# Kernel optimization log

Measured on AMD Instinct MI355X. Metric: run time of the kernel, lower is better.

## Reference

```python
import jax, jax.numpy as jnp
import numpy as np

E, B, S, D, F = 8, 2, 1024, 1024, 4096


def setup_inputs() -> dict:
    key = jax.random.key(0)
    ks = jax.random.split(key, 9)
    sc_d = 1.0 / np.sqrt(D)
    sc_f = 1.0 / np.sqrt(F)
    hidden_states = jax.random.normal(ks[0], (B, S, D), dtype=jnp.float32)
    # router outputs set externally on the parent model in the original code
    gating_probs = jax.nn.softmax(jax.random.normal(ks[1], (B, E), dtype=jnp.float32), axis=-1)
    shared_gate_prob = jax.nn.sigmoid(jax.random.normal(ks[2], (B, 1), dtype=jnp.float32))
    # stacked expert SwiGLU MLP weights (Llama-style gate/up/down)
    Wg = jax.random.normal(ks[3], (E, D, F), dtype=jnp.float32) * sc_d
    Wu = jax.random.normal(ks[4], (E, D, F), dtype=jnp.float32) * sc_d
    Wd = jax.random.normal(ks[5], (E, F, D), dtype=jnp.float32) * sc_f
    # shared expert MLP
    Sg = jax.random.normal(ks[6], (D, F), dtype=jnp.float32) * sc_d
    Su = jax.random.normal(ks[7], (D, F), dtype=jnp.float32) * sc_d
    Sd = jax.random.normal(ks[8], (F, D), dtype=jnp.float32) * sc_f
    return {
        "hidden_states": hidden_states,
        "gating_probs": gating_probs,
        "shared_gate_prob": shared_gate_prob,
        "Wg": Wg, "Wu": Wu, "Wd": Wd,
        "Sg": Sg, "Su": Su, "Sd": Sd,
    }


def reference(hidden_states, gating_probs, shared_gate_prob, Wg, Wu, Wd, Sg, Su, Sd):
    h = hidden_states  # [B,S,D]
    # every expert's MLP runs on all tokens (naive all-experts-dense, as in source)
    g = jnp.einsum("bsd,edf->ebsf", h, Wg)
    u = jnp.einsum("bsd,edf->ebsf", h, Wu)
    expert_outs = jnp.einsum("ebsf,efd->ebsd", jax.nn.silu(g) * u, Wd)  # [E,B,S,D]
    # weighted_sum routing with per-sequence gating probs [B,E]
    expert_output = jnp.einsum("be,ebsd->bsd", gating_probs, expert_outs)
    # shared expert MLP
    shared = jnp.einsum("bsf,fd->bsd", jax.nn.silu(h @ Sg) * (h @ Su), Sd)
    sg = shared_gate_prob[:, :, None]  # [B,1,1]
    return (1.0 - sg) * expert_output + sg * shared
```

## Files before the change

### kernel.cpp

```cpp
#include <hip/hip_runtime.h>
#include <cstdio>
#include <cstdint>

typedef _Float16 f16;
typedef _Float16 f16x4 __attribute__((ext_vector_type(4)));
typedef _Float16 f16x8 __attribute__((ext_vector_type(8)));
typedef float f32x4 __attribute__((ext_vector_type(4)));

#define GLL16(gp, lp)                                                          \
  __builtin_amdgcn_global_load_lds(                                            \
      (const __attribute__((address_space(1))) void*)(gp),                     \
      (__attribute__((address_space(3))) void*)(lp), 16, 0, 0)

#define BARX __builtin_amdgcn_s_barrier()
#define WAITV4 { asm volatile("s_waitcnt vmcnt(4)" ::: "memory"); __builtin_amdgcn_sched_barrier(0); }
#define WAITV0 { asm volatile("s_waitcnt vmcnt(0)" ::: "memory"); __builtin_amdgcn_sched_barrier(0); }
#define WAITL0 { asm volatile("s_waitcnt lgkmcnt(0)" ::: "memory"); __builtin_amdgcn_sched_barrier(0); }

__global__ void cvt_f32_f16_kernel(const float* __restrict__ in,
                                   f16* __restrict__ out, int n4) {
  int i = blockIdx.x * blockDim.x + threadIdx.x;
  if (i < n4) {
    f32x4 v = reinterpret_cast<const f32x4*>(in)[i];
    f16x4 o;
    o[0] = (f16)v[0]; o[1] = (f16)v[1]; o[2] = (f16)v[2]; o[3] = (f16)v[3];
    reinterpret_cast<f16x4*>(out)[i] = o;
  }
}

__global__ void tr_cvt2_kernel(const float* __restrict__ inA,
                               const float* __restrict__ inB,
                               f16* __restrict__ out, size_t slotOff,
                               int C, size_t OS, int nA) {
  int slot = blockIdx.z;
  const float* src = (slot < nA) ? inA + (size_t)slot * 64 * gridDim.y * C : inB;
  f16* dst = out + (size_t)slot * slotOff;
  __shared__ f16 tl[4096];
  int t = threadIdx.x;
  int r0 = blockIdx.y * 64, c0 = blockIdx.x * 64;
  int br = (t >> 4) * 4, bc = (t & 15) * 4;
  f32x4 v[4];
#pragma unroll
  for (int i = 0; i < 4; ++i)
    v[i] = *(const f32x4*)&src[(size_t)(r0 + br + i) * C + c0 + bc];
#pragma unroll
  for (int cc = 0; cc < 4; ++cc) {
    int c = bc + cc;
    f16x4 o;
    o[0] = (f16)v[0][cc]; o[1] = (f16)v[1][cc];
    o[2] = (f16)v[2][cc]; o[3] = (f16)v[3][cc];
    *(f16x4*)&tl[c * 64 + (br ^ ((c & 7) * 8))] = o;
  }
  __syncthreads();
  int rw = (t & 7) * 8, cw = t >> 3;
#pragma unroll
  for (int j = 0; j < 2; ++j) {
    int c = cw + j * 32;
    f16x8 o = *(const f16x8*)&tl[c * 64 + (rw ^ ((c & 7) * 8))];
    *(f16x8*)&dst[(size_t)(c0 + c) * OS + r0 + rw] = o;
  }
}

#define STAGE_A5(tile, hf)                                                     \
  do {                                                                         \
    const f16* g_ = Abase + (size_t)((hf) * 128) * 1024 + (tile) * 64 + aVoff; \
    f16* d_ = &lds[(2 * ((tile) & 1) + (hf)) * 8192 + w * 512];                \
    GLL16(g_, d_);                                                             \
    GLL16(g_ + (size_t)64 * 1024, d_ + 4096);                                  \
  } while (0)
#define STAGE_G5(tile)                                                         \
  do {                                                                         \
    const f16* g_ = Gbase + (tile) * 64 + aVoff;                               \
    f16* d_ = &lds[32768 + (2 * ((tile) & 1)) * 8192 + w * 512];               \
    GLL16(g_, d_);                                                             \
    GLL16(g_ + (size_t)64 * 1024, d_ + 4096);                                  \
  } while (0)
#define STAGE_U5(tile)                                                         \
  do {                                                                         \
    const f16* g_ = Ubase + (tile) * 64 + aVoff;                               \
    f16* d_ = &lds[32768 + (2 * ((tile) & 1) + 1) * 8192 + w * 512];           \
    GLL16(g_, d_);                                                             \
    GLL16(g_ + (size_t)64 * 1024, d_ + 4096);                                  \
  } while (0)

#define RD_A5(rh, buf)                                                         \
  do {                                                                         \
    const f16* p_ = &lds[(2 * (buf) + wr) * 8192 + (rh) * 4096];               \
    aFd[0][0] = *(const f16x8*)(p_ + 0 * 1024 + vR0);                          \
    aFd[0][1] = *(const f16x8*)(p_ + 0 * 1024 + vR1);                          \
    aFd[1][0] = *(const f16x8*)(p_ + 1 * 1024 + vR0);                          \
    aFd[1][1] = *(const f16x8*)(p_ + 1 * 1024 + vR1);                          \
    aFd[2][0] = *(const f16x8*)(p_ + 2 * 1024 + vR0);                          \
    aFd[2][1] = *(const f16x8*)(p_ + 2 * 1024 + vR1);                          \
    aFd[3][0] = *(const f16x8*)(p_ + 3 * 1024 + vR0);                          \
    aFd[3][1] = *(const f16x8*)(p_ + 3 * 1024 + vR1);                          \
  } while (0)
#define RD_B5(ch, buf)                                                         \
  do {                                                                         \
    const f16* p_ = &lds[32768 + (2 * (buf) + bh) * 8192 + bq * 4096 +         \
                         (ch) * 2 * 1024];                                     \
    bFd[(ch) * 2][0] = *(const f16x8*)(p_ + vR0);                              \
    bFd[(ch) * 2][1] = *(const f16x8*)(p_ + vR1);                              \
    bFd[(ch) * 2 + 1][0] = *(const f16x8*)(p_ + 1024 + vR0);                   \
    bFd[(ch) * 2 + 1][1] = *(const f16x8*)(p_ + 1024 + vR1);                   \
  } while (0)

#define MFMA165(rh, ch)                                                        \
  do {                                                                         \
    __builtin_amdgcn_s_setprio(1);                                             \
    _Pragma("unroll") for (int rt = 0; rt < 4; ++rt)                           \
        _Pragma("unroll") for (int ct = 0; ct < 2; ++ct)                       \
        _Pragma("unroll") for (int ks = 0; ks < 2; ++ks)                       \
            acc[(rh) * 4 + rt][(ch) * 2 + ct] =                                \
        __builtin_amdgcn_mfma_f32_16x16x32_f16(                                \
            aFd[rt][ks], bFd[(ch) * 2 + ct][ks],                               \
            acc[(rh) * 4 + rt][(ch) * 2 + ct], 0, 0, 0);                       \
    __builtin_amdgcn_s_setprio(0);                                             \
    __builtin_amdgcn_sched_barrier(0);                                         \
  } while (0)

__global__ __launch_bounds__(512, 2) void gemmUG5_kernel(
    const f16* __restrict__ A, const f16* __restrict__ Bg,
    const f16* __restrict__ Bu, f16* __restrict__ T,
    const float* __restrict__ gate, const float* __restrict__ sgp) {
  __shared__ __align__(16) f16 lds[65536];

  int lgl = (blockIdx.x & 7) * 288 + (blockIdx.x >> 3);
  int mt = lgl & 7;
  int ntg = lgl >> 3;
  int slot = ntg >> 5;
  int ntl = ntg & 31;

  int t = threadIdx.x, w = t >> 6, l = t & 63;
  int wr = w >> 2, wc = w & 3;
  int bh = wc >> 1, bq = wc & 1;

  int scol = (((l & 7) ^ ((l >> 3) & 7)) * 8);
  size_t aVoff = (size_t)(w * 8 + (l >> 3)) * 1024 + scol;
  const f16* Abase = A + (size_t)mt * 256 * 1024;
  const f16* Gbase = Bg + (size_t)slot * 4194304 + (size_t)ntl * 128 * 1024;
  const f16* Ubase = Bu + (size_t)slot * 4194304 + (size_t)ntl * 128 * 1024;

  int vR0 = (l & 15) * 64 + (((l >> 4) * 8) ^ ((l & 7) * 8));
  int vR1 = (l & 15) * 64 + ((32 + (l >> 4) * 8) ^ ((l & 7) * 8));

  f16x8 aFd[4][2], bFd[4][2];
  f32x4 acc[8][4] = {};

  STAGE_G5(0); STAGE_U5(0);
  STAGE_A5(0, 0); STAGE_A5(0, 1);
  STAGE_G5(1); STAGE_U5(1);
  WAITV4;
  BARX;

#pragma unroll 1
  for (int it = 0; it < 7; ++it) {
    int t1 = 2 * it + 1, t2 = 2 * it + 2, t3 = 2 * it + 3;
    RD_A5(0, 0); RD_B5(0, 0); STAGE_A5(t1, 0);
    BARX; WAITL0; MFMA165(0, 0); BARX;
    RD_B5(1, 0); STAGE_A5(t1, 1);
    BARX; WAITL0; MFMA165(0, 1); BARX;
    RD_A5(1, 0); STAGE_G5(t2);
    BARX; WAITL0; MFMA165(1, 0); BARX;
    STAGE_U5(t2);
    BARX; MFMA165(1, 1); WAITV4; BARX;
    RD_A5(0, 1); RD_B5(0, 1); STAGE_A5(t2, 0);
    BARX; WAITL0; MFMA165(0, 0); BARX;
    RD_B5(1, 1); STAGE_A5(t2, 1);
    BARX; WAITL0; MFMA165(0, 1); BARX;
    RD_A5(1, 1); STAGE_G5(t3);
    BARX; WAITL0; MFMA165(1, 0); BARX;
    STAGE_U5(t3);
    BARX; MFMA165(1, 1); WAITV4; BARX;
  }
  RD_A5(0, 0); RD_B5(0, 0); STAGE_A5(15, 0);
  BARX; WAITL0; MFMA165(0, 0); BARX;
  RD_B5(1, 0); STAGE_A5(15, 1);
  BARX; WAITL0; MFMA165(0, 1); BARX;
  RD_A5(1, 0);
  BARX; WAITL0; MFMA165(1, 0); BARX;
  BARX; MFMA165(1, 1); WAITV0; BARX;
  RD_A5(0, 1); RD_B5(0, 1);
  BARX; WAITL0; MFMA165(0, 0); BARX;
  RD_B5(1, 1);
  BARX; WAITL0; MFMA165(0, 1); BARX;
  RD_A5(1, 1);
  BARX; WAITL0; MFMA165(1, 0); BARX;
  MFMA165(1, 1);

  int r0 = (l >> 4) * 4, c0 = l & 15;
  float* xf = (float*)lds;
  if (wc >= 2) {
    float* wb = xf + (wr * 2 + (wc - 2)) * 8192 + l * 128;
#pragma unroll
    for (int rt = 0; rt < 8; ++rt)
#pragma unroll
      for (int ct = 0; ct < 4; ++ct)
        *(f32x4*)(wb + ((rt ^ (l & 7)) * 16 + ct * 4)) = acc[rt][ct];
  }
  WAITL0;
  BARX;
  if (wc < 2) {
    const float* rb = xf + (wr * 2 + wc) * 8192 + l * 128;
    int rowb = mt * 256 + wr * 128;
    size_t colb = (size_t)ntg * 128 + wc * 64;
    int b = mt >> 2;
    float s = sgp[b];
    float coef = (slot < 8) ? (1.f - s) * gate[b * 8 + slot] : s;
#pragma unroll
    for (int rt = 0; rt < 8; ++rt) {
#pragma unroll
      for (int ct = 0; ct < 4; ++ct) {
        f32x4 uv = *(const f32x4*)(rb + ((rt ^ (l & 7)) * 16 + ct * 4));
#pragma unroll
        for (int j = 0; j < 4; ++j) {
          float g = acc[rt][ct][j];
          float u = uv[j];
          T[(size_t)(rowb + rt * 16 + r0 + j) * 36864 + colb + ct * 16 + c0] =
              (f16)(g / (1.f + __expf(-g)) * u * coef);
        }
      }
    }
  }
}

#define STAGE_A(tile, hf)                                                      \
  do {                                                                         \
    const f16* g_ = Abase + (size_t)((hf) * 128) * LD + (tile) * 64 + aVoff;   \
    f16* d_ = &lds[(2 * ((tile) & 1) + (hf)) * 8192 + w * 512];                \
    GLL16(g_, d_);                                                             \
    GLL16(g_ + (size_t)64 * LD, d_ + 4096);                                    \
  } while (0)
#define STAGE_B(tile, hf)                                                      \
  do {                                                                         \
    const f16* g_ = Bbase + (size_t)((hf) * 128) * LD + (tile) * 64 + aVoff;   \
    f16* d_ = &lds[32768 + (2 * ((tile) & 1) + (hf)) * 8192 + w * 512];        \
    GLL16(g_, d_);                                                             \
    GLL16(g_ + (size_t)64 * LD, d_ + 4096);                                    \
  } while (0)

#define RD_A(rh, buf)                                                          \
  do {                                                                         \
    const f16* p_ = &lds[(2 * (buf) + wr) * 8192 + (rh) * 4096];               \
    aFd[0][0] = *(const f16x8*)(p_ + 0 * 1024 + vR0);                          \
    aFd[0][1] = *(const f16x8*)(p_ + 0 * 1024 + vR1);                          \
    aFd[1][0] = *(const f16x8*)(p_ + 1 * 1024 + vR0);                          \
    aFd[1][1] = *(const f16x8*)(p_ + 1 * 1024 + vR1);                          \
    aFd[2][0] = *(const f16x8*)(p_ + 2 * 1024 + vR0);                          \
    aFd[2][1] = *(const f16x8*)(p_ + 2 * 1024 + vR1);                          \
    aFd[3][0] = *(const f16x8*)(p_ + 3 * 1024 + vR0);                          \
    aFd[3][1] = *(const f16x8*)(p_ + 3 * 1024 + vR1);                          \
  } while (0)
#define RD_B(ch, buf)                                                          \
  do {                                                                         \
    const f16* p_ = &lds[32768 + (2 * (buf) + bh) * 8192 + bq * 4096 +         \
                         (ch) * 2 * 1024];                                     \
    bFd[(ch) * 2][0] = *(const f16x8*)(p_ + vR0);                              \
    bFd[(ch) * 2][1] = *(const f16x8*)(p_ + vR1);                              \
    bFd[(ch) * 2 + 1][0] = *(const f16x8*)(p_ + 1024 + vR0);                   \
    bFd[(ch) * 2 + 1][1] = *(const f16x8*)(p_ + 1024 + vR1);                   \
  } while (0)

#define MFMA16(rh, ch)                                                         \
  do {                                                                         \
    __builtin_amdgcn_s_setprio(1);                                             \
    _Pragma("unroll") for (int rt = 0; rt < 4; ++rt)                           \
        _Pragma("unroll") for (int ct = 0; ct < 2; ++ct)                       \
        _Pragma("unroll") for (int ks = 0; ks < 2; ++ks)                       \
            acc[(rh) * 4 + rt][(ch) * 2 + ct] =                                \
        __builtin_amdgcn_mfma_f32_16x16x32_f16(                                \
            aFd[rt][ks], bFd[(ch) * 2 + ct][ks],                               \
            acc[(rh) * 4 + rt][(ch) * 2 + ct], 0, 0, 0);                       \
    __builtin_amdgcn_s_setprio(0);                                             \
    __builtin_amdgcn_sched_barrier(0);                                         \
  } while (0)

__global__ __launch_bounds__(512, 2) void gemmD_kernel(
    const f16* __restrict__ A, const f16* __restrict__ B,
    float* __restrict__ P) {
  constexpr size_t LD = 36864;
  constexpr int NTILES = 72;
  __shared__ __align__(16) f16 lds[65536];

  int wg = (blockIdx.x & 7) * 32 + (blockIdx.x >> 3);
  int kpart = wg >> 5, mt = (wg >> 2) & 7, nt = wg & 3;

  int t = threadIdx.x, w = t >> 6, l = t & 63;
  int wr = w >> 2, wc = w & 3;
  int bh = wc >> 1, bq = wc & 1;

  int scol = (((l & 7) ^ ((l >> 3) & 7)) * 8);
  size_t stRow = (size_t)(w * 8 + (l >> 3)) * LD;
  size_t aVoff = stRow + scol;
  const f16* Abase = A + (size_t)mt * 256 * LD + (size_t)kpart * 4608;
  const f16* Bbase = B + (size_t)nt * 256 * LD + (size_t)kpart * 4608;

  int vR0 = (l & 15) * 64 + (((l >> 4) * 8) ^ ((l & 7) * 8));
  int vR1 = (l & 15) * 64 + ((32 + (l >> 4) * 8) ^ ((l & 7) * 8));

  f16x8 aFd[4][2], bFd[4][2];
  f32x4 acc[8][4] = {};

  STAGE_B(0, 0); STAGE_B(0, 1);
  STAGE_A(0, 0); STAGE_A(0, 1);
  STAGE_B(1, 0); STAGE_B(1, 1);
  WAITV4;
  BARX;

#pragma unroll 1
  for (int it = 0; it < NTILES / 2 - 1; ++it) {
    int t1 = 2 * it + 1, t2 = 2 * it + 2, t3 = 2 * it + 3;
    RD_A(0, 0); RD_B(0, 0); STAGE_A(t1, 0);
    BARX; WAITL0; MFMA16(0, 0); BARX;
    RD_B(1, 0); STAGE_A(t1, 1);
    BARX; WAITL0; MFMA16(0, 1); BARX;
    RD_A(1, 0); STAGE_B(t2, 0);
    BARX; WAITL0; MFMA16(1, 0); BARX;
    STAGE_B(t2, 1);
    BARX; MFMA16(1, 1); WAITV4; BARX;
    RD_A(0, 1); RD_B(0, 1); STAGE_A(t2, 0);
    BARX; WAITL0; MFMA16(0, 0); BARX;
    RD_B(1, 1); STAGE_A(t2, 1);
    BARX; WAITL0; MFMA16(0, 1); BARX;
    RD_A(1, 1); STAGE_B(t3, 0);
    BARX; WAITL0; MFMA16(1, 0); BARX;
    STAGE_B(t3, 1);
    BARX; MFMA16(1, 1); WAITV4; BARX;
  }
  RD_A(0, 0); RD_B(0, 0); STAGE_A(NTILES - 1, 0);
  BARX; WAITL0; MFMA16(0, 0); BARX;
  RD_B(1, 0); STAGE_A(NTILES - 1, 1);
  BARX; WAITL0; MFMA16(0, 1); BARX;
  RD_A(1, 0);
  BARX; WAITL0; MFMA16(1, 0); BARX;
  BARX; MFMA16(1, 1); WAITV0; BARX;
  RD_A(0, 1); RD_B(0, 1);
  BARX; WAITL0; MFMA16(0, 0); BARX;
  RD_B(1, 1);
  BARX; WAITL0; MFMA16(0, 1); BARX;
  RD_A(1, 1);
  BARX; WAITL0; MFMA16(1, 0); BARX;
  MFMA16(1, 1);

  int r0 = (l >> 4) * 4, c0 = l & 15;
  size_t base = ((size_t)kpart << 21);
  int rowbase = mt * 256 + wr * 128;
  int colbase = nt * 256 + wc * 64;
#pragma unroll
  for (int rt = 0; rt < 8; ++rt)
#pragma unroll
    for (int ct = 0; ct < 4; ++ct)
#pragma unroll
      for (int j = 0; j < 4; ++j)
        P[base + (size_t)(rowbase + rt * 16 + r0 + j) * 1024 + colbase +
          ct * 16 + c0] = acc[rt][ct][j];
}

__global__ void reduce8_kernel(const float* __restrict__ P,
                               float* __restrict__ out, int n4) {
  int i = blockIdx.x * blockDim.x + threadIdx.x;
  if (i < n4) {
    f32x4 s = {0.f, 0.f, 0.f, 0.f};
#pragma unroll
    for (int e = 0; e < 8; ++e) {
      f32x4 v = reinterpret_cast<const f32x4*>(P + ((size_t)e << 21))[i];
      s += v;
    }
    reinterpret_cast<f32x4*>(out)[i] = s;
  }
}

extern "C" void kernel_launch(void* const* d_in, const int* in_sizes, int n_in,
                              void* d_out, int out_size, void* d_ws,
                              size_t ws_size, hipStream_t stream) {
  const float* h    = (const float*)d_in[0];
  const float* gate = (const float*)d_in[1];
  const float* sgp  = (const float*)d_in[2];
  const float* Wg   = (const float*)d_in[3];
  const float* Wu   = (const float*)d_in[4];
  const float* Wd   = (const float*)d_in[5];
  const float* Sg   = (const float*)d_in[6];
  const float* Su   = (const float*)d_in[7];
  const float* Sd   = (const float*)d_in[8];

  const size_t SZ_HB = 4194304;
  const size_t SZ_W  = 75497472;
  const size_t SZ_T  = 150994944;
  const size_t SZ_P  = 67108864;
  char* ws = (char*)d_ws;
  f16*   hb  = (f16*)(ws);
  f16*   WgT = (f16*)(ws + SZ_HB);
  f16*   WuT = (f16*)(ws + SZ_HB + SZ_W);
  f16*   WdT = (f16*)(ws + SZ_HB + 2 * SZ_W);
  f16*   T   = (f16*)(ws + SZ_HB + 3 * SZ_W);
  float* P   = (float*)(ws + SZ_HB + 3 * SZ_W + SZ_T);
  size_t need = SZ_HB + 3 * SZ_W + SZ_T + SZ_P;
  if (ws_size < need) {
    fprintf(stderr, "kernel_launch: ws too small (%zu < %zu)\n", ws_size, need);
    return;
  }
  float* out = (float*)d_out;

  cvt_f32_f16_kernel<<<2048, 256, 0, stream>>>(h, hb, 524288);
  tr_cvt2_kernel<<<dim3(64, 16, 9), 256, 0, stream>>>(
      Wg, Sg, WgT, 4096ull * 1024, 4096, 1024, 8);
  tr_cvt2_kernel<<<dim3(64, 16, 9), 256, 0, stream>>>(
      Wu, Su, WuT, 4096ull * 1024, 4096, 1024, 8);
  tr_cvt2_kernel<<<dim3(16, 64, 9), 256, 0, stream>>>(
      Wd, Sd, WdT, 4096, 1024, 36864, 8);

  gemmUG5_kernel<<<2304, 512, 0, stream>>>(hb, WgT, WuT, T, gate, sgp);
  gemmD_kernel<<<256, 512, 0, stream>>>(T, WdT, P);
  reduce8_kernel<<<2048, 256, 0, stream>>>(P, out, 524288);
}
```

Baseline: 613.7 us.

## Make up/gate GEMM persistent over nine tiles and store split-K partials in fp16

```diff
diff --git a/kernel.cpp b/kernel.cpp
--- a/kernel.cpp
+++ b/kernel.cpp
@@ -61,21 +61,21 @@
   }
 }
 
-#define STAGE_A5(tile, hf)                                                     \
+#define STAGE_A8(tile, hf)                                                     \
   do {                                                                         \
     const f16* g_ = Abase + (size_t)((hf) * 128) * 1024 + (tile) * 64 + aVoff; \
     f16* d_ = &lds[(2 * ((tile) & 1) + (hf)) * 8192 + w * 512];                \
     GLL16(g_, d_);                                                             \
     GLL16(g_ + (size_t)64 * 1024, d_ + 4096);                                  \
   } while (0)
-#define STAGE_G5(tile)                                                         \
+#define STAGE_G8(tile)                                                         \
   do {                                                                         \
     const f16* g_ = Gbase + (tile) * 64 + aVoff;                               \
     f16* d_ = &lds[32768 + (2 * ((tile) & 1)) * 8192 + w * 512];               \
     GLL16(g_, d_);                                                             \
     GLL16(g_ + (size_t)64 * 1024, d_ + 4096);                                  \
   } while (0)
-#define STAGE_U5(tile)                                                         \
+#define STAGE_U8(tile)                                                         \
   do {                                                                         \
     const f16* g_ = Ubase + (tile) * 64 + aVoff;                               \
     f16* d_ = &lds[32768 + (2 * ((tile) & 1) + 1) * 8192 + w * 512];           \
@@ -83,7 +83,7 @@
     GLL16(g_ + (size_t)64 * 1024, d_ + 4096);                                  \
   } while (0)
 
-#define RD_A5(rh, buf)                                                         \
+#define RD_A8(rh, buf)                                                         \
   do {                                                                         \
     const f16* p_ = &lds[(2 * (buf) + wr) * 8192 + (rh) * 4096];               \
     aFd[0][0] = *(const f16x8*)(p_ + 0 * 1024 + vR0);                          \
@@ -95,7 +95,7 @@
     aFd[3][0] = *(const f16x8*)(p_ + 3 * 1024 + vR0);                          \
     aFd[3][1] = *(const f16x8*)(p_ + 3 * 1024 + vR1);                          \
   } while (0)
-#define RD_B5(ch, buf)                                                         \
+#define RD_B8(ch, buf)                                                         \
   do {                                                                         \
     const f16* p_ = &lds[32768 + (2 * (buf) + bh) * 8192 + bq * 4096 +         \
                          (ch) * 2 * 1024];                                     \
@@ -105,7 +105,7 @@
     bFd[(ch) * 2 + 1][1] = *(const f16x8*)(p_ + 1024 + vR1);                   \
   } while (0)
 
-#define MFMA165(rh, ch)                                                        \
+#define MFMA8(rh, ch)                                                          \
   do {                                                                         \
     __builtin_amdgcn_s_setprio(1);                                             \
     _Pragma("unroll") for (int rt = 0; rt < 4; ++rt)                           \
@@ -119,17 +119,16 @@
     __builtin_amdgcn_sched_barrier(0);                                         \
   } while (0)
 
-__global__ __launch_bounds__(512, 2) void gemmUG5_kernel(
+__global__ __launch_bounds__(512, 2) void gemmUG8_kernel(
     const f16* __restrict__ A, const f16* __restrict__ Bg,
     const f16* __restrict__ Bu, f16* __restrict__ T,
     const float* __restrict__ gate, const float* __restrict__ sgp) {
   __shared__ __align__(16) f16 lds[65536];
 
-  int lgl = (blockIdx.x & 7) * 288 + (blockIdx.x >> 3);
-  int mt = lgl & 7;
-  int ntg = lgl >> 3;
-  int slot = ntg >> 5;
-  int ntl = ntg & 31;
+  int xcd = blockIdx.x & 7;
+  int idx = blockIdx.x >> 3;
+  int mt = idx & 7;
+  int q = xcd * 4 + (idx >> 3);
 
   int t = threadIdx.x, w = t >> 6, l = t & 63;
   int wr = w >> 2, wc = w & 3;
@@ -138,8 +137,6 @@
   int scol = (((l & 7) ^ ((l >> 3) & 7)) * 8);
   size_t aVoff = (size_t)(w * 8 + (l >> 3)) * 1024 + scol;
   const f16* Abase = A + (size_t)mt * 256 * 1024;
-  const f16* Gbase = Bg + (size_t)slot * 4194304 + (size_t)ntl * 128 * 1024;
-  const f16* Ubase = Bu + (size_t)slot * 4194304 + (size_t)ntl * 128 * 1024;
 
   int vR0 = (l & 15) * 64 + (((l >> 4) * 8) ^ ((l & 7) * 8));
   int vR1 = (l & 15) * 64 + ((32 + (l >> 4) * 8) ^ ((l & 7) * 8));
@@ -147,80 +144,98 @@
   f16x8 aFd[4][2], bFd[4][2];
   f32x4 acc[8][4] = {};
 
-  STAGE_G5(0); STAGE_U5(0);
-  STAGE_A5(0, 0); STAGE_A5(0, 1);
-  STAGE_G5(1); STAGE_U5(1);
-  WAITV4;
-  BARX;
+  int r0 = (l >> 4) * 4, c0 = l & 15;
+  int rowb = mt * 256 + wr * 128;
+  float sgv = sgp[mt >> 2];
+  float* xf = (float*)lds;
 
 #pragma unroll 1
-  for (int it = 0; it < 7; ++it) {
-    int t1 = 2 * it + 1, t2 = 2 * it + 2, t3 = 2 * it + 3;
-    RD_A5(0, 0); RD_B5(0, 0); STAGE_A5(t1, 0);
-    BARX; WAITL0; MFMA165(0, 0); BARX;
-    RD_B5(1, 0); STAGE_A5(t1, 1);
-    BARX; WAITL0; MFMA165(0, 1); BARX;
-    RD_A5(1, 0); STAGE_G5(t2);
-    BARX; WAITL0; MFMA165(1, 0); BARX;
-    STAGE_U5(t2);
-    BARX; MFMA165(1, 1); WAITV4; BARX;
-    RD_A5(0, 1); RD_B5(0, 1); STAGE_A5(t2, 0);
-    BARX; WAITL0; MFMA165(0, 0); BARX;
-    RD_B5(1, 1); STAGE_A5(t2, 1);
-    BARX; WAITL0; MFMA165(0, 1); BARX;
-    RD_A5(1, 1); STAGE_G5(t3);
-    BARX; WAITL0; MFMA165(1, 0); BARX;
-    STAGE_U5(t3);
-    BARX; MFMA165(1, 1); WAITV4; BARX;
-  }
-  RD_A5(0, 0); RD_B5(0, 0); STAGE_A5(15, 0);
-  BARX; WAITL0; MFMA165(0, 0); BARX;
-  RD_B5(1, 0); STAGE_A5(15, 1);
-  BARX; WAITL0; MFMA165(0, 1); BARX;
-  RD_A5(1, 0);
-  BARX; WAITL0; MFMA165(1, 0); BARX;
-  BARX; MFMA165(1, 1); WAITV0; BARX;
-  RD_A5(0, 1); RD_B5(0, 1);
-  BARX; WAITL0; MFMA165(0, 0); BARX;
-  RD_B5(1, 1);
-  BARX; WAITL0; MFMA165(0, 1); BARX;
-  RD_A5(1, 1);
-  BARX; WAITL0; MFMA165(1, 0); BARX;
-  MFMA165(1, 1);
-
-  int r0 = (l >> 4) * 4, c0 = l & 15;
-  float* xf = (float*)lds;
-  if (wc >= 2) {
-    float* wb = xf + (wr * 2 + (wc - 2)) * 8192 + l * 128;
-#pragma unroll
-    for (int rt = 0; rt < 8; ++rt)
-#pragma unroll
-      for (int ct = 0; ct < 4; ++ct)
-        *(f32x4*)(wb + ((rt ^ (l & 7)) * 16 + ct * 4)) = acc[rt][ct];
-  }
-  WAITL0;
-  BARX;
-  if (wc < 2) {
-    const float* rb = xf + (wr * 2 + wc) * 8192 + l * 128;
-    int rowb = mt * 256 + wr * 128;
-    size_t colb = (size_t)ntg * 128 + wc * 64;
-    int b = mt >> 2;
-    float s = sgp[b];
-    float coef = (slot < 8) ? (1.f - s) * gate[b * 8 + slot] : s;
-#pragma unroll
-    for (int rt = 0; rt < 8; ++rt) {
-#pragma unroll
-      for (int ct = 0; ct < 4; ++ct) {
-        f32x4 uv = *(const f32x4*)(rb + ((rt ^ (l & 7)) * 16 + ct * 4));
-#pragma unroll
-        for (int j = 0; j < 4; ++j) {
-          float g = acc[rt][ct][j];
-          float u = uv[j];
-          T[(size_t)(rowb + rt * 16 + r0 + j) * 36864 + colb + ct * 16 + c0] =
-              (f16)(g / (1.f + __expf(-g)) * u * coef);
+  for (int s = 0; s < 9; ++s) {
+    int ntg = q * 9 + s;
+    int slot = ntg >> 5;
+    int ntl = ntg & 31;
+    const f16* Gbase = Bg + (size_t)slot * 4194304 + (size_t)ntl * 128 * 1024;
+    const f16* Ubase = Bu + (size_t)slot * 4194304 + (size_t)ntl * 128 * 1024;
+
+    STAGE_G8(0); STAGE_U8(0);
+    STAGE_A8(0, 0); STAGE_A8(0, 1);
+    STAGE_G8(1); STAGE_U8(1);
+    WAITV4;
+    BARX;
+
+#pragma unroll 1
+    for (int it = 0; it < 7; ++it) {
+      int t1 = 2 * it + 1, t2 = 2 * it + 2, t3 = 2 * it + 3;
+      RD_A8(0, 0); RD_B8(0, 0); STAGE_A8(t1, 0);
+      BARX; WAITL0; MFMA8(0, 0); BARX;
+      RD_B8(1, 0); STAGE_A8(t1, 1);
+      BARX; WAITL0; MFMA8(0, 1); BARX;
+      RD_A8(1, 0); STAGE_G8(t2);
+      BARX; WAITL0; MFMA8(1, 0); BARX;
+      STAGE_U8(t2);
+      BARX; MFMA8(1, 1); WAITV4; BARX;
+      RD_A8(0, 1); RD_B8(0, 1); STAGE_A8(t2, 0);
+      BARX; WAITL0; MFMA8(0, 0); BARX;
+      RD_B8(1, 1); STAGE_A8(t2, 1);
+      BARX; WAITL0; MFMA8(0, 1); BARX;
+      RD_A8(1, 1); STAGE_G8(t3);
+      BARX; WAITL0; MFMA8(1, 0); BARX;
+      STAGE_U8(t3);
+      BARX; MFMA8(1, 1); WAITV4; BARX;
+    }
+    RD_A8(0, 0); RD_B8(0, 0); STAGE_A8(15, 0);
+    BARX; WAITL0; MFMA8(0, 0); BARX;
+    RD_B8(1, 0); STAGE_A8(15, 1);
+    BARX; WAITL0; MFMA8(0, 1); BARX;
+    RD_A8(1, 0);
+    BARX; WAITL0; MFMA8(1, 0); BARX;
+    BARX; MFMA8(1, 1); WAITV0; BARX;
+    RD_A8(0, 1); RD_B8(0, 1);
+    BARX; WAITL0; MFMA8(0, 0); BARX;
+    RD_B8(1, 1);
+    BARX; WAITL0; MFMA8(0, 1); BARX;
+    RD_A8(1, 1);
+    BARX; WAITL0; MFMA8(1, 0); BARX;
+    MFMA8(1, 1);
+
+    if (bh == 1) {
+      float* wb = xf + (wr * 2 + bq) * 8192 + l * 128;
+#pragma unroll
+      for (int rt = 0; rt < 8; ++rt)
+#pragma unroll
+        for (int ct = 0; ct < 4; ++ct) {
+          int idx2 = rt * 4 + ct;
+          *(f32x4*)(wb + (((idx2 + l) & 31) * 4)) = acc[rt][ct];
+        }
+    }
+    WAITL0;
+    BARX;
+    if (bh == 0) {
+      const float* rb = xf + (wr * 2 + bq) * 8192 + l * 128;
+      size_t colb = (size_t)ntg * 128 + bq * 64;
+      float coef = (slot < 8) ? (1.f - sgv) * gate[(mt >> 2) * 8 + slot] : sgv;
+#pragma unroll
+      for (int rt = 0; rt < 8; ++rt) {
+#pragma unroll
+        for (int ct = 0; ct < 4; ++ct) {
+          int idx2 = rt * 4 + ct;
+          f32x4 uv = *(const f32x4*)(rb + (((idx2 + l) & 31) * 4));
+#pragma unroll
+          for (int j = 0; j < 4; ++j) {
+            float g = acc[rt][ct][j];
+            T[(size_t)(rowb + rt * 16 + r0 + j) * 36864 + colb + ct * 16 +
+              c0] = (f16)(g / (1.f + __expf(-g)) * uv[j] * coef);
+          }
         }
       }
     }
+    WAITL0;
+    BARX;
+#pragma unroll
+    for (int rt = 0; rt < 8; ++rt)
+#pragma unroll
+      for (int ct = 0; ct < 4; ++ct)
+        acc[rt][ct] = (f32x4){0.f, 0.f, 0.f, 0.f};
   }
 }
 
@@ -277,7 +292,7 @@
 
 __global__ __launch_bounds__(512, 2) void gemmD_kernel(
     const f16* __restrict__ A, const f16* __restrict__ B,
-    float* __restrict__ P) {
+    f16* __restrict__ P) {
   constexpr size_t LD = 36864;
   constexpr int NTILES = 72;
   __shared__ __align__(16) f16 lds[65536];
@@ -353,18 +368,19 @@
 #pragma unroll
       for (int j = 0; j < 4; ++j)
         P[base + (size_t)(rowbase + rt * 16 + r0 + j) * 1024 + colbase +
-          ct * 16 + c0] = acc[rt][ct][j];
-}
-
-__global__ void reduce8_kernel(const float* __restrict__ P,
+          ct * 16 + c0] = (f16)acc[rt][ct][j];
+}
+
+__global__ void reduce8_kernel(const f16* __restrict__ P,
                                float* __restrict__ out, int n4) {
   int i = blockIdx.x * blockDim.x + threadIdx.x;
   if (i < n4) {
     f32x4 s = {0.f, 0.f, 0.f, 0.f};
 #pragma unroll
     for (int e = 0; e < 8; ++e) {
-      f32x4 v = reinterpret_cast<const f32x4*>(P + ((size_t)e << 21))[i];
-      s += v;
+      f16x4 v = reinterpret_cast<const f16x4*>(P + ((size_t)e << 21))[i];
+      s[0] += (float)v[0]; s[1] += (float)v[1];
+      s[2] += (float)v[2]; s[3] += (float)v[3];
     }
     reinterpret_cast<f32x4*>(out)[i] = s;
   }
@@ -386,14 +402,14 @@
   const size_t SZ_HB = 4194304;
   const size_t SZ_W  = 75497472;
   const size_t SZ_T  = 150994944;
-  const size_t SZ_P  = 67108864;
+  const size_t SZ_P  = 33554432;
   char* ws = (char*)d_ws;
   f16*   hb  = (f16*)(ws);
   f16*   WgT = (f16*)(ws + SZ_HB);
   f16*   WuT = (f16*)(ws + SZ_HB + SZ_W);
   f16*   WdT = (f16*)(ws + SZ_HB + 2 * SZ_W);
   f16*   T   = (f16*)(ws + SZ_HB + 3 * SZ_W);
-  float* P   = (float*)(ws + SZ_HB + 3 * SZ_W + SZ_T);
+  f16*   P   = (f16*)(ws + SZ_HB + 3 * SZ_W + SZ_T);
   size_t need = SZ_HB + 3 * SZ_W + SZ_T + SZ_P;
   if (ws_size < need) {
     fprintf(stderr, "kernel_launch: ws too small (%zu < %zu)\n", ws_size, need);
@@ -409,7 +425,7 @@
   tr_cvt2_kernel<<<dim3(16, 64, 9), 256, 0, stream>>>(
       Wd, Sd, WdT, 4096, 1024, 36864, 8);
 
-  gemmUG5_kernel<<<2304, 512, 0, stream>>>(hb, WgT, WuT, T, gate, sgp);
+  gemmUG8_kernel<<<256, 512, 0, stream>>>(hb, WgT, WuT, T, gate, sgp);
   gemmD_kernel<<<256, 512, 0, stream>>>(T, WdT, P);
   reduce8_kernel<<<2048, 256, 0, stream>>>(P, out, 524288);
 }
```

Measured after the change: 704.0 us. 1.15x slower.
